# Kernel tuning notes

Hardware: AMD Instinct MI355X
Metric: run time of the kernel (lower is better)

The kernel has to match this reference:

```python
import jax, jax.numpy as jnp
import numpy as np

B, IN, OUT, HS, NBDA = 128, 256, 256, 512, 1

def setup_inputs() -> dict:
    key = jax.random.key(0)
    ks = jax.random.split(key, 16)
    d = {}
    d["inputs"] = jax.random.normal(ks[0], (B, IN), dtype=jnp.float32)
    d["hidden"] = jax.random.normal(ks[1], (B, HS), dtype=jnp.float32)
    d["hebb"] = jax.random.normal(ks[2], (B, HS, HS), dtype=jnp.float32) * 0.1
    # learned params (torch.nn.Linear: y = x @ W.T + b)
    d["i2h_w"] = jax.random.normal(ks[3], (HS, IN), dtype=jnp.float32) * (1.0 / np.sqrt(IN))
    d["i2h_b"] = jnp.zeros((HS,), dtype=jnp.float32)
    d["w"] = 0.01 * jax.random.uniform(ks[4], (HS, HS), dtype=jnp.float32)
    d["alpha"] = 0.01 * jax.random.uniform(ks[5], (HS, HS), dtype=jnp.float32)
    d["h2o_w"] = jax.random.normal(ks[6], (OUT, HS), dtype=jnp.float32) * (1.0 / np.sqrt(HS))
    d["h2o_b"] = jnp.zeros((OUT,), dtype=jnp.float32)
    d["h2v_w"] = jax.random.normal(ks[7], (1, HS), dtype=jnp.float32) * (1.0 / np.sqrt(HS))
    d["h2v_b"] = jnp.zeros((1,), dtype=jnp.float32)
    d["h2da_w"] = jax.random.normal(ks[8], (NBDA, HS), dtype=jnp.float32) * (1.0 / np.sqrt(HS))
    d["h2da_b"] = jnp.zeros((NBDA,), dtype=jnp.float32)
    return d

def reference(inputs, hidden, hebb, i2h_w, i2h_b, w, alpha, h2o_w, h2o_b,
              h2v_w, h2v_b, h2da_w, h2da_b):
    # hactiv = tanh(i2h(x) + (w + alpha*hebb) @ hidden), per-sample weight matrix
    pre = inputs @ i2h_w.T + i2h_b                              # [B, HS]
    w_eff = w + alpha * hebb                                    # [B, HS, HS]
    rec = jnp.einsum('bij,bj->bi', w_eff, hidden)               # [B, HS]
    hactiv = jnp.tanh(pre + rec)                                # [B, HS]
    activout = hactiv @ h2o_w.T + h2o_b                         # [B, OUT]
    valueout = hactiv @ h2v_w.T + h2v_b                         # [B, 1]
    da = jnp.tanh(hactiv @ h2da_w.T + h2da_b)                   # [B, NBDA]
    # outer-product Hebbian update, DA-modulated, clamped to [-1, 1]
    deltahebb = hactiv[:, :, None] * hidden[:, None, :]         # [B, HS, HS]
    hebb_new = jnp.clip(hebb + da[:, :1, None] * deltahebb, -1.0, 1.0)
    return activout, valueout, hactiv, hebb_new
```

## Files before the change

### kernel.cpp

```cpp
#include <hip/hip_runtime.h>
#include <cstddef>
#include <cstdint>

#define B_    128
#define IN_   256
#define OUT_  256
#define HS_   512

#define NTHR_  512
#define NBLK_  1024
#define SPLIT_ 8

__device__ __forceinline__ float clip1(float x) {
    return fminf(fmaxf(x, -1.f), 1.f);
}

__global__ __launch_bounds__(NTHR_, 4) void fused_stream(
    const float* __restrict__ inputs,
    const float* __restrict__ hidden,
    const float* __restrict__ hebb,
    const float* __restrict__ i2h_w,
    const float* __restrict__ i2h_b,
    const float* __restrict__ w,
    const float* __restrict__ alpha,
    const float* __restrict__ h2o_w,
    const float* __restrict__ h2o_b,
    const float* __restrict__ h2v_w,
    const float* __restrict__ h2v_b,
    const float* __restrict__ h2da_w,
    const float* __restrict__ h2da_b,
    float* __restrict__ activout,
    float* __restrict__ valueout,
    float* __restrict__ hactiv,
    float* __restrict__ hebb_new,
    float* __restrict__ ws_pd,
    float* __restrict__ ws_pv,
    int*   __restrict__ ws_cnt)
{
    const int blk  = blockIdx.x;
    const int b    = blk >> 3;
    const int s    = blk & 7;
    const int tid  = threadIdx.x;
    const int wave = tid >> 6;
    const int lane = tid & 63;
    const int r0   = s * 64 + wave * 8;
    const int lr0  = wave * 8;

    __shared__ float s_hrow[64];
    __shared__ float s_pd[8], s_pv[8];
    __shared__ float s_bc[2];
    __shared__ float s_h[HS_];
    __shared__ float s_part[512];

    const float4* hid4 = (const float4*)(hidden + (size_t)b * HS_);
    const float4 h0  = hid4[lane];
    const float4 h1  = hid4[lane + 64];
    const float4 in4 = ((const float4*)(inputs + (size_t)b * IN_))[lane];

    const float4* hb4 = (const float4*)hebb + ((size_t)b * HS_) * (HS_ / 4);
    const float4* w4  = (const float4*)w;
    const float4* a4  = (const float4*)alpha;
    const float4* iw4 = (const float4*)i2h_w;

    float pd = 0.f, pv = 0.f;
    for (int t = 0; t < 8; t += 2) {
        const int i = r0 + t;
        const float4* hpA = hb4 + (size_t)i * (HS_ / 4);
        const float4* hpB = hpA + (HS_ / 4);
        const float4* wpA = w4  + (size_t)i * (HS_ / 4);
        const float4* apA = a4  + (size_t)i * (HS_ / 4);
        const float4* ipA = iw4 + (size_t)i * (IN_ / 4);

        const float4 xA0 = hpA[lane],            xA1 = hpA[lane + 64];
        const float4 xB0 = hpB[lane],            xB1 = hpB[lane + 64];
        const float4 wA0 = wpA[lane],            wA1 = wpA[lane + 64];
        const float4 wB0 = wpA[128 + lane],      wB1 = wpA[128 + lane + 64];
        const float4 aA0 = apA[lane],            aA1 = apA[lane + 64];
        const float4 aB0 = apA[128 + lane],      aB1 = apA[128 + lane + 64];
        const float4 iA  = ipA[lane];
        const float4 iB  = ipA[64 + lane];

        float a, c;
        a  = (wA0.x + aA0.x * xA0.x) * h0.x;
        a += (wA0.y + aA0.y * xA0.y) * h0.y;
        a += (wA0.z + aA0.z * xA0.z) * h0.z;
        a += (wA0.w + aA0.w * xA0.w) * h0.w;
        a += (wA1.x + aA1.x * xA1.x) * h1.x;
        a += (wA1.y + aA1.y * xA1.y) * h1.y;
        a += (wA1.z + aA1.z * xA1.z) * h1.z;
        a += (wA1.w + aA1.w * xA1.w) * h1.w;
        a += iA.x * in4.x + iA.y * in4.y + iA.z * in4.z + iA.w * in4.w;

        c  = (wB0.x + aB0.x * xB0.x) * h0.x;
        c += (wB0.y + aB0.y * xB0.y) * h0.y;
        c += (wB0.z + aB0.z * xB0.z) * h0.z;
        c += (wB0.w + aB0.w * xB0.w) * h0.w;
        c += (wB1.x + aB1.x * xB1.x) * h1.x;
        c += (wB1.y + aB1.y * xB1.y) * h1.y;
        c += (wB1.z + aB1.z * xB1.z) * h1.z;
        c += (wB1.w + aB1.w * xB1.w) * h1.w;
        c += iB.x * in4.x + iB.y * in4.y + iB.z * in4.z + iB.w * in4.w;

        #pragma unroll
        for (int off = 1; off < 64; off <<= 1) {
            a += __shfl_xor(a, off, 64);
            c += __shfl_xor(c, off, 64);
        }

        const float hA = tanhf(a + i2h_b[i]);
        const float hB = tanhf(c + i2h_b[i + 1]);
        if (lane == 0) {
            s_hrow[lr0 + t]     = hA;
            s_hrow[lr0 + t + 1] = hB;
            float2* hp = (float2*)(hactiv + (size_t)b * HS_ + i);
            *hp = make_float2(hA, hB);
            pd += hA * h2da_w[i] + hB * h2da_w[i + 1];
            pv += hA * h2v_w[i]  + hB * h2v_w[i + 1];
        }
    }

    if (lane == 0) { s_pd[wave] = pd; s_pv[wave] = pv; }
    __syncthreads();

    if (tid == 0) {
        float sd = 0.f, sv = 0.f;
        #pragma unroll
        for (int k = 0; k < 8; ++k) { sd += s_pd[k]; sv += s_pv[k]; }
        __hip_atomic_fetch_add(&ws_pd[b], sd, __ATOMIC_RELAXED,
                               __HIP_MEMORY_SCOPE_AGENT);
        __hip_atomic_fetch_add(&ws_pv[b], sv, __ATOMIC_RELAXED,
                               __HIP_MEMORY_SCOPE_AGENT);
        __hip_atomic_fetch_add(&ws_cnt[b], 1, __ATOMIC_RELEASE,
                               __HIP_MEMORY_SCOPE_AGENT);
        while (__hip_atomic_load(&ws_cnt[b], __ATOMIC_ACQUIRE,
                                 __HIP_MEMORY_SCOPE_AGENT) < SPLIT_)
            __builtin_amdgcn_s_sleep(1);
        const float pdt = __hip_atomic_load(&ws_pd[b], __ATOMIC_RELAXED,
                                            __HIP_MEMORY_SCOPE_AGENT);
        const float pvt = __hip_atomic_load(&ws_pv[b], __ATOMIC_RELAXED,
                                            __HIP_MEMORY_SCOPE_AGENT);
        s_bc[0] = tanhf(pdt + h2da_b[0]);
        s_bc[1] = pvt + h2v_b[0];
    }
    __syncthreads();
    const float da_b = s_bc[0];
    if (s == 0 && tid == 0)
        valueout[b] = s_bc[1];

    for (int t = 0; t < 8; t += 2) {
        const int i = r0 + t;
        const float4* xp = hb4 + (size_t)i * (HS_ / 4);
        const float4 x0 = xp[lane],       x1 = xp[lane + 64];
        const float4 y0 = xp[128 + lane], y1 = xp[128 + lane + 64];
        const float scA = da_b * s_hrow[lr0 + t];
        const float scB = da_b * s_hrow[lr0 + t + 1];

        float4 o0, o1, p0, p1;
        o0.x = clip1(fmaf(scA, h0.x, x0.x));
        o0.y = clip1(fmaf(scA, h0.y, x0.y));
        o0.z = clip1(fmaf(scA, h0.z, x0.z));
        o0.w = clip1(fmaf(scA, h0.w, x0.w));
        o1.x = clip1(fmaf(scA, h1.x, x1.x));
        o1.y = clip1(fmaf(scA, h1.y, x1.y));
        o1.z = clip1(fmaf(scA, h1.z, x1.z));
        o1.w = clip1(fmaf(scA, h1.w, x1.w));
        p0.x = clip1(fmaf(scB, h0.x, y0.x));
        p0.y = clip1(fmaf(scB, h0.y, y0.y));
        p0.z = clip1(fmaf(scB, h0.z, y0.z));
        p0.w = clip1(fmaf(scB, h0.w, y0.w));
        p1.x = clip1(fmaf(scB, h1.x, y1.x));
        p1.y = clip1(fmaf(scB, h1.y, y1.y));
        p1.z = clip1(fmaf(scB, h1.z, y1.z));
        p1.w = clip1(fmaf(scB, h1.w, y1.w));

        float4* dp = (float4*)hebb_new + ((size_t)b * HS_ + i) * (HS_ / 4);
        dp[lane]            = o0;
        dp[lane + 64]       = o1;
        dp[128 + lane]      = p0;
        dp[128 + lane + 64] = p1;
    }

    if (tid < 128)
        ((float4*)s_h)[tid] = ((const float4*)(hactiv + (size_t)b * HS_))[tid];
    __syncthreads();

    {
        const int ol = tid & 31;
        const int sg = tid >> 5;
        const int o  = s * 32 + ol;
        const float4* wp  = (const float4*)(h2o_w + (size_t)o * HS_);
        const float4* hp4 = (const float4*)s_h;
        float acc = 0.f;
        #pragma unroll
        for (int c2 = 0; c2 < 8; ++c2) {
            const float4 wv = wp[sg * 8 + c2];
            const float4 hv = hp4[sg * 8 + c2];
            acc += wv.x * hv.x + wv.y * hv.y + wv.z * hv.z + wv.w * hv.w;
        }
        s_part[sg * 32 + ol] = acc;
    }
    __syncthreads();
    if (tid < 32) {
        const int o = s * 32 + tid;
        float acc = h2o_b[o];
        #pragma unroll
        for (int k = 0; k < 16; ++k)
            acc += s_part[k * 32 + tid];
        activout[(size_t)b * OUT_ + o] = acc;
    }
}

__global__ __launch_bounds__(256) void k1_hactiv(
    const float* __restrict__ inputs, const float* __restrict__ hidden,
    const float* __restrict__ hebb, const float* __restrict__ i2h_w,
    const float* __restrict__ i2h_b, const float* __restrict__ w,
    const float* __restrict__ alpha, float* __restrict__ hactiv)
{
    const int b     = blockIdx.x & (B_ - 1);
    const int chunk = blockIdx.x >> 7;
    const int tid   = threadIdx.x;
    const int wave  = tid >> 6;
    const int lane  = tid & 63;

    const float4* hid4 = (const float4*)(hidden + (size_t)b * HS_);
    const float4  h0   = hid4[lane];
    const float4  h1   = hid4[lane + 64];
    const float4  in4  = ((const float4*)(inputs + (size_t)b * IN_))[lane];

    const int i0 = chunk * 64 + wave * 16;

    for (int r = 0; r < 16; ++r) {
        const int i = i0 + r;
        const float4* hb = (const float4*)(hebb + ((size_t)b * HS_ + i) * HS_);
        const float4* wr = (const float4*)(w     + (size_t)i * HS_);
        const float4* ar = (const float4*)(alpha + (size_t)i * HS_);

        const float4 hb0 = hb[lane];
        const float4 hb1 = hb[lane + 64];
        const float4 wv0 = wr[lane];
        const float4 wv1 = wr[lane + 64];
        const float4 av0 = ar[lane];
        const float4 av1 = ar[lane + 64];
        const float4 iw  = ((const float4*)(i2h_w + (size_t)i * IN_))[lane];

        float acc;
        acc  = (wv0.x + av0.x * hb0.x) * h0.x;
        acc += (wv0.y + av0.y * hb0.y) * h0.y;
        acc += (wv0.z + av0.z * hb0.z) * h0.z;
        acc += (wv0.w + av0.w * hb0.w) * h0.w;
        acc += (wv1.x + av1.x * hb1.x) * h1.x;
        acc += (wv1.y + av1.y * hb1.y) * h1.y;
        acc += (wv1.z + av1.z * hb1.z) * h1.z;
        acc += (wv1.w + av1.w * hb1.w) * h1.w;
        acc += iw.x * in4.x + iw.y * in4.y + iw.z * in4.z + iw.w * in4.w;

        #pragma unroll
        for (int off = 32; off > 0; off >>= 1)
            acc += __shfl_down(acc, off, 64);

        if (lane == 0)
            hactiv[(size_t)b * HS_ + i] = tanhf(acc + i2h_b[i]);
    }
}

__global__ __launch_bounds__(256) void k2_heads(
    const float* __restrict__ hactiv, const float* __restrict__ h2o_w,
    const float* __restrict__ h2o_b, const float* __restrict__ h2v_w,
    const float* __restrict__ h2v_b, const float* __restrict__ h2da_w,
    const float* __restrict__ h2da_b, float* __restrict__ activout,
    float* __restrict__ valueout, float* __restrict__ da)
{
    const int b   = blockIdx.x;
    const int tid = threadIdx.x;

    __shared__ float s_h[HS_];
    __shared__ float red_v[256];
    __shared__ float red_d[256];

    for (int t = tid; t < HS_; t += 256)
        s_h[t] = hactiv[(size_t)b * HS_ + t];
    __syncthreads();

    const float4* wr  = (const float4*)(h2o_w + (size_t)tid * HS_);
    const float4* sh4 = (const float4*)s_h;
    float acc = 0.f;
    #pragma unroll 4
    for (int q = 0; q < HS_ / 4; ++q) {
        const float4 wv = wr[q];
        const float4 hv = sh4[q];
        acc += wv.x * hv.x + wv.y * hv.y + wv.z * hv.z + wv.w * hv.w;
    }
    activout[(size_t)b * OUT_ + tid] = acc + h2o_b[tid];

    float pv = 0.f, pd = 0.f;
    for (int t = tid; t < HS_; t += 256) {
        const float hv = s_h[t];
        pv += hv * h2v_w[t];
        pd += hv * h2da_w[t];
    }
    red_v[tid] = pv;
    red_d[tid] = pd;
    __syncthreads();
    for (int s2 = 128; s2 > 0; s2 >>= 1) {
        if (tid < s2) {
            red_v[tid] += red_v[tid + s2];
            red_d[tid] += red_d[tid + s2];
        }
        __syncthreads();
    }
    if (tid == 0) {
        valueout[b] = red_v[0] + h2v_b[0];
        da[b]       = tanhf(red_d[0] + h2da_b[0]);
    }
}

__global__ __launch_bounds__(256) void k3_hebb(
    const float* __restrict__ hebb, const float* __restrict__ hidden,
    const float* __restrict__ hactiv, const float* __restrict__ da,
    float* __restrict__ hebb_new)
{
    const int tid = threadIdx.x;
    const size_t base = (size_t)blockIdx.x * 1024;

    #pragma unroll
    for (int k = 0; k < 4; ++k) {
        const size_t idx = base + (size_t)k * 256 + tid;
        const int j4  = (int)(idx & 127);
        const int row = (int)(idx >> 7);
        const int i   = row & (HS_ - 1);
        const int b   = row >> 9;

        const float scale = da[b] * hactiv[(size_t)b * HS_ + i];
        const float4 hv = ((const float4*)hebb)[idx];
        const float4 hd = ((const float4*)hidden)[(size_t)b * (HS_ / 4) + j4];

        float4 r;
        r.x = fminf(fmaxf(fmaf(scale, hd.x, hv.x), -1.f), 1.f);
        r.y = fminf(fmaxf(fmaf(scale, hd.y, hv.y), -1.f), 1.f);
        r.z = fminf(fmaxf(fmaf(scale, hd.z, hv.z), -1.f), 1.f);
        r.w = fminf(fmaxf(fmaf(scale, hd.w, hv.w), -1.f), 1.f);
        ((float4*)hebb_new)[idx] = r;
    }
}

extern "C" void kernel_launch(void* const* d_in, const int* in_sizes, int n_in,
                              void* d_out, int out_size, void* d_ws, size_t ws_size,
                              hipStream_t stream)
{
    const float* inputs = (const float*)d_in[0];
    const float* hidden = (const float*)d_in[1];
    const float* hebb   = (const float*)d_in[2];
    const float* i2h_w  = (const float*)d_in[3];
    const float* i2h_b  = (const float*)d_in[4];
    const float* w      = (const float*)d_in[5];
    const float* alpha  = (const float*)d_in[6];
    const float* h2o_w  = (const float*)d_in[7];
    const float* h2o_b  = (const float*)d_in[8];
    const float* h2v_w  = (const float*)d_in[9];
    const float* h2v_b  = (const float*)d_in[10];
    const float* h2da_w = (const float*)d_in[11];
    const float* h2da_b = (const float*)d_in[12];

    float* out = (float*)d_out;
    float* activout = out;
    float* valueout = out + 32768;
    float* hactiv   = out + 32768 + 128;
    float* hebb_new = out + 32768 + 128 + 65536;

    const size_t gate_bytes = (size_t)(3 * B_) * sizeof(float);

    int maxb = 0;
    hipError_t oe = hipOccupancyMaxActiveBlocksPerMultiprocessor(
        &maxb, fused_stream, NTHR_, 0);

    if (ws_size >= gate_bytes && oe == hipSuccess && maxb >= 4) {
        float* ws_pd  = (float*)d_ws;
        float* ws_pv  = ws_pd + B_;
        int*   ws_cnt = (int*)(ws_pv + B_);

        hipMemsetAsync(d_ws, 0, gate_bytes, stream);

        fused_stream<<<dim3(NBLK_), dim3(NTHR_), 0, stream>>>(
            inputs, hidden, hebb, i2h_w, i2h_b, w, alpha,
            h2o_w, h2o_b, h2v_w, h2v_b, h2da_w, h2da_b,
            activout, valueout, hactiv, hebb_new,
            ws_pd, ws_pv, ws_cnt);
    } else {
        float* da = (float*)d_ws;
        k1_hactiv<<<dim3(1024), dim3(256), 0, stream>>>(
            inputs, hidden, hebb, i2h_w, i2h_b, w, alpha, hactiv);
        k2_heads<<<dim3(B_), dim3(256), 0, stream>>>(
            hactiv, h2o_w, h2o_b, h2v_w, h2v_b, h2da_w, h2da_b,
            activout, valueout, da);
        k3_hebb<<<dim3(8192), dim3(256), 0, stream>>>(
            hebb, hidden, hactiv, da, hebb_new);
    }
}
```

Measured before the change: 299.7 us.

## Split fused kernel into two passes, replacing the spin barrier, and use nontemporal stores

Replaces the single fused kernel, which used atomic counters and a spin-wait gate per batch row, with two kernel launches. The first computes hactiv and writes per-block partial sums for the da and value heads. The second reduces those partials and does the Hebbian update and output head. This removes the memset, the atomics and the spin-wait, and writes hebb_new with nontemporal stores. The cost is a second launch and a second read of hebb, because the fused version likely found its rows still in cache after the first pass.

```diff
diff --git a/kernel.cpp b/kernel.cpp
--- a/kernel.cpp
+++ b/kernel.cpp
@@ -9,13 +9,17 @@
 
 #define NTHR_  512
 #define NBLK_  1024
-#define SPLIT_ 8
 
 __device__ __forceinline__ float clip1(float x) {
     return fminf(fmaxf(x, -1.f), 1.f);
 }
 
-__global__ __launch_bounds__(NTHR_, 4) void fused_stream(
+typedef float f32x4 __attribute__((ext_vector_type(4)));
+__device__ __forceinline__ void nt_store4(float4* p, float4 v) {
+    __builtin_nontemporal_store(*(f32x4*)&v, (f32x4*)p);
+}
+
+__global__ __launch_bounds__(NTHR_, 4) void k_pass1(
     const float* __restrict__ inputs,
     const float* __restrict__ hidden,
     const float* __restrict__ hebb,
@@ -23,19 +27,11 @@
     const float* __restrict__ i2h_b,
     const float* __restrict__ w,
     const float* __restrict__ alpha,
-    const float* __restrict__ h2o_w,
-    const float* __restrict__ h2o_b,
     const float* __restrict__ h2v_w,
-    const float* __restrict__ h2v_b,
     const float* __restrict__ h2da_w,
-    const float* __restrict__ h2da_b,
-    float* __restrict__ activout,
-    float* __restrict__ valueout,
     float* __restrict__ hactiv,
-    float* __restrict__ hebb_new,
     float* __restrict__ ws_pd,
-    float* __restrict__ ws_pv,
-    int*   __restrict__ ws_cnt)
+    float* __restrict__ ws_pv)
 {
     const int blk  = blockIdx.x;
     const int b    = blk >> 3;
@@ -44,13 +40,8 @@
     const int wave = tid >> 6;
     const int lane = tid & 63;
     const int r0   = s * 64 + wave * 8;
-    const int lr0  = wave * 8;
-
-    __shared__ float s_hrow[64];
+
     __shared__ float s_pd[8], s_pv[8];
-    __shared__ float s_bc[2];
-    __shared__ float s_h[HS_];
-    __shared__ float s_part[512];
 
     const float4* hid4 = (const float4*)(hidden + (size_t)b * HS_);
     const float4 h0  = hid4[lane];
@@ -110,8 +101,6 @@
         const float hA = tanhf(a + i2h_b[i]);
         const float hB = tanhf(c + i2h_b[i + 1]);
         if (lane == 0) {
-            s_hrow[lr0 + t]     = hA;
-            s_hrow[lr0 + t + 1] = hB;
             float2* hp = (float2*)(hactiv + (size_t)b * HS_ + i);
             *hp = make_float2(hA, hB);
             pd += hA * h2da_w[i] + hB * h2da_w[i + 1];
@@ -121,39 +110,70 @@
 
     if (lane == 0) { s_pd[wave] = pd; s_pv[wave] = pv; }
     __syncthreads();
-
     if (tid == 0) {
         float sd = 0.f, sv = 0.f;
         #pragma unroll
         for (int k = 0; k < 8; ++k) { sd += s_pd[k]; sv += s_pv[k]; }
-        __hip_atomic_fetch_add(&ws_pd[b], sd, __ATOMIC_RELAXED,
-                               __HIP_MEMORY_SCOPE_AGENT);
-        __hip_atomic_fetch_add(&ws_pv[b], sv, __ATOMIC_RELAXED,
-                               __HIP_MEMORY_SCOPE_AGENT);
-        __hip_atomic_fetch_add(&ws_cnt[b], 1, __ATOMIC_RELEASE,
-                               __HIP_MEMORY_SCOPE_AGENT);
-        while (__hip_atomic_load(&ws_cnt[b], __ATOMIC_ACQUIRE,
-                                 __HIP_MEMORY_SCOPE_AGENT) < SPLIT_)
-            __builtin_amdgcn_s_sleep(1);
-        const float pdt = __hip_atomic_load(&ws_pd[b], __ATOMIC_RELAXED,
-                                            __HIP_MEMORY_SCOPE_AGENT);
-        const float pvt = __hip_atomic_load(&ws_pv[b], __ATOMIC_RELAXED,
-                                            __HIP_MEMORY_SCOPE_AGENT);
-        s_bc[0] = tanhf(pdt + h2da_b[0]);
-        s_bc[1] = pvt + h2v_b[0];
+        ws_pd[b * 8 + s] = sd;
+        ws_pv[b * 8 + s] = sv;
+    }
+}
+
+__global__ __launch_bounds__(NTHR_, 4) void k_pass2(
+    const float* __restrict__ hidden,
+    const float* __restrict__ hebb,
+    const float* __restrict__ h2o_w,
+    const float* __restrict__ h2o_b,
+    const float* __restrict__ h2v_b,
+    const float* __restrict__ h2da_b,
+    const float* __restrict__ hactiv,
+    float* __restrict__ activout,
+    float* __restrict__ valueout,
+    float* __restrict__ hebb_new,
+    const float* __restrict__ ws_pd,
+    const float* __restrict__ ws_pv)
+{
+    const int blk  = blockIdx.x;
+    const int b    = blk >> 3;
+    const int s    = blk & 7;
+    const int tid  = threadIdx.x;
+    const int wave = tid >> 6;
+    const int lane = tid & 63;
+    const int r0   = s * 64 + wave * 8;
+
+    __shared__ float s_h[HS_];
+    __shared__ float s_part[512];
+    __shared__ float s_bc[1];
+
+    if (tid < 128)
+        ((float4*)s_h)[tid] = ((const float4*)(hactiv + (size_t)b * HS_))[tid];
+    if (tid == 0) {
+        float sd = 0.f, sv = 0.f;
+        #pragma unroll
+        for (int k = 0; k < 8; ++k) {
+            sd += ws_pd[b * 8 + k];
+            sv += ws_pv[b * 8 + k];
+        }
+        s_bc[0] = tanhf(sd + h2da_b[0]);
+        if (s == 0)
+            valueout[b] = sv + h2v_b[0];
     }
     __syncthreads();
     const float da_b = s_bc[0];
-    if (s == 0 && tid == 0)
-        valueout[b] = s_bc[1];
+
+    const float4* hid4 = (const float4*)(hidden + (size_t)b * HS_);
+    const float4 h0 = hid4[lane];
+    const float4 h1 = hid4[lane + 64];
+
+    const float4* hb4 = (const float4*)hebb + ((size_t)b * HS_) * (HS_ / 4);
 
     for (int t = 0; t < 8; t += 2) {
         const int i = r0 + t;
         const float4* xp = hb4 + (size_t)i * (HS_ / 4);
         const float4 x0 = xp[lane],       x1 = xp[lane + 64];
         const float4 y0 = xp[128 + lane], y1 = xp[128 + lane + 64];
-        const float scA = da_b * s_hrow[lr0 + t];
-        const float scB = da_b * s_hrow[lr0 + t + 1];
+        const float scA = da_b * s_h[i];
+        const float scB = da_b * s_h[i + 1];
 
         float4 o0, o1, p0, p1;
         o0.x = clip1(fmaf(scA, h0.x, x0.x));
@@ -174,15 +194,11 @@
         p1.w = clip1(fmaf(scB, h1.w, y1.w));
 
         float4* dp = (float4*)hebb_new + ((size_t)b * HS_ + i) * (HS_ / 4);
-        dp[lane]            = o0;
-        dp[lane + 64]       = o1;
-        dp[128 + lane]      = p0;
-        dp[128 + lane + 64] = p1;
-    }
-
-    if (tid < 128)
-        ((float4*)s_h)[tid] = ((const float4*)(hactiv + (size_t)b * HS_))[tid];
-    __syncthreads();
+        nt_store4(dp + lane,            o0);
+        nt_store4(dp + lane + 64,       o1);
+        nt_store4(dp + 128 + lane,      p0);
+        nt_store4(dp + 128 + lane + 64, p1);
+    }
 
     {
         const int ol = tid & 31;
@@ -367,24 +383,19 @@
     float* hactiv   = out + 32768 + 128;
     float* hebb_new = out + 32768 + 128 + 65536;
 
-    const size_t gate_bytes = (size_t)(3 * B_) * sizeof(float);
-
-    int maxb = 0;
-    hipError_t oe = hipOccupancyMaxActiveBlocksPerMultiprocessor(
-        &maxb, fused_stream, NTHR_, 0);
-
-    if (ws_size >= gate_bytes && oe == hipSuccess && maxb >= 4) {
-        float* ws_pd  = (float*)d_ws;
-        float* ws_pv  = ws_pd + B_;
-        int*   ws_cnt = (int*)(ws_pv + B_);
-
-        hipMemsetAsync(d_ws, 0, gate_bytes, stream);
-
-        fused_stream<<<dim3(NBLK_), dim3(NTHR_), 0, stream>>>(
+    const size_t part_bytes = (size_t)(2 * B_ * 8) * sizeof(float);
+
+    if (ws_size >= part_bytes) {
+        float* ws_pd = (float*)d_ws;
+        float* ws_pv = ws_pd + B_ * 8;
+
+        k_pass1<<<dim3(NBLK_), dim3(NTHR_), 0, stream>>>(
             inputs, hidden, hebb, i2h_w, i2h_b, w, alpha,
-            h2o_w, h2o_b, h2v_w, h2v_b, h2da_w, h2da_b,
-            activout, valueout, hactiv, hebb_new,
-            ws_pd, ws_pv, ws_cnt);
+            h2v_w, h2da_w, hactiv, ws_pd, ws_pv);
+
+        k_pass2<<<dim3(NBLK_), dim3(NTHR_), 0, stream>>>(
+            hidden, hebb, h2o_w, h2o_b, h2v_b, h2da_b,
+            hactiv, activout, valueout, hebb_new, ws_pd, ws_pv);
     } else {
         float* da = (float*)d_ws;
         k1_hactiv<<<dim3(1024), dim3(256), 0, stream>>>(
```

Result: faster. 285.5 us (-4.7%).
